# Optimization experiments

Hardware: AMD Instinct MI355X
Metric: run time of the kernel (lower is better)

The kernel has to match this reference:

```python
import jax, jax.numpy as jnp
import numpy as np

N = 50000
L = 3


def gcn_conv(x, W, b, src, dst):
    """PyG-style GCNConv: add self-loops, symmetric deg^-1/2 normalization,
    linear transform, scatter-add aggregation at destination nodes."""
    loops = jnp.arange(N, dtype=src.dtype)
    s = jnp.concatenate([src, loops])  # [E+N]
    d = jnp.concatenate([dst, loops])
    deg = jax.ops.segment_sum(jnp.ones(s.shape[0], x.dtype), d, num_segments=N)
    dinv = jnp.where(deg > 0, jax.lax.rsqrt(deg), jnp.zeros_like(deg))
    norm = dinv[s] * dinv[d]  # [E+N]
    xw = x @ W  # [N, F_out]
    out = jax.ops.segment_sum(xw[s] * norm[:, None], d, num_segments=N)
    return out + b


def setup_inputs() -> dict:
    key = jax.random.key(0)
    ks = jax.random.split(key, 6)
    E = 1600000
    F_in, F_hid, F_out = 256, 128, 64
    x = jax.random.normal(ks[0], (N, F_in), dtype=jnp.float32)
    edges = jax.random.randint(ks[1], (L, 2, E), 0, N, dtype=jnp.int32)
    W1 = jax.random.normal(ks[2], (L, F_in, F_hid), dtype=jnp.float32) * (1.0 / np.sqrt(F_in))
    b1 = jnp.zeros((L, F_hid), dtype=jnp.float32)
    W2 = jax.random.normal(ks[3], (L, F_hid, F_out), dtype=jnp.float32) * (1.0 / np.sqrt(F_hid))
    b2 = jnp.zeros((L, F_out), dtype=jnp.float32)
    return {"x": x, "edges": edges, "W1": W1, "b1": b1, "W2": W2, "b2": b2}


def reference(x, edges, W1, b1, W2, b2):
    # layer 1: sum of L GCNConvs over the L rewired graphs
    h = jnp.zeros((N, W1.shape[2]), dtype=x.dtype)
    for i in range(L):
        h = h + gcn_conv(x, W1[i], b1[i], edges[i, 0], edges[i, 1])
    h = jax.nn.relu(h)
    # layer 2
    out = jnp.zeros((N, W2.shape[2]), dtype=x.dtype)
    for i in range(L):
        out = out + gcn_conv(h, W2[i], b2[i], edges[i, 0], edges[i, 1])
    return out
```

## Files before the change

### kernel.cpp

```cpp
#include <hip/hip_runtime.h>

typedef unsigned int uint;
typedef unsigned short ushort;

#define NN 50000
#define NE 1600000
#define NL 3
#define NB 782
#define CAP 2560
#define CHUNK 8192

typedef float f32x4 __attribute__((ext_vector_type(4)));
typedef __bf16 bf16x4v __attribute__((ext_vector_type(4)));
typedef __bf16 bf16x8v __attribute__((ext_vector_type(8)));

__device__ __forceinline__ ushort f2bf(float f) {
    uint u = __float_as_uint(f);
    u += 0x7fffu + ((u >> 16) & 1u);
    return (ushort)(u >> 16);
}
__device__ __forceinline__ float bf2f(uint lo16) { return __uint_as_float(lo16 << 16); }

__global__ void zero_k(int* __restrict__ p, int n) {
    int i = blockIdx.x * 256 + threadIdx.x;
    if (i < n) p[i] = 0;
}

__global__ void cvt_w(const float* __restrict__ W1, const float* __restrict__ W2,
                      ushort* __restrict__ w1t, ushort* __restrict__ w2t) {
    int idx = blockIdx.x * 256 + threadIdx.x;
    const int n1 = NL * 256 * 128;
    const int n2 = NL * 128 * 64;
    if (idx < n1) {
        int i = idx / (128 * 256);
        int rem = idx % (128 * 256);
        int c = rem / 256, k = rem % 256;
        w1t[idx] = f2bf(W1[i * 256 * 128 + k * 128 + c]);
    } else if (idx < n1 + n2) {
        int j = idx - n1;
        int i = j / (64 * 128);
        int rem = j % (64 * 128);
        int c = rem / 128, k = rem % 128;
        w2t[j] = f2bf(W2[i * 128 * 64 + k * 64 + c]);
    }
}

__global__ __launch_bounds__(256) void bin_edges(const int* __restrict__ edges,
                                                 int* __restrict__ gcur,
                                                 uint* __restrict__ bins) {
    __shared__ uint hist[NB];
    __shared__ uint base[NB];
    const int t = threadIdx.x;
    const int g = blockIdx.y;
    const int e0 = blockIdx.x * CHUNK;
    const int n = min(CHUNK, NE - e0);
    const int* srcp = edges + (size_t)g * 2 * NE;
    const int* dstp = srcp + NE;

    for (int b = t; b < NB; b += 256) hist[b] = 0u;
    __syncthreads();
    for (int k = t; k < n; k += 256) {
        int dst = dstp[e0 + k];
        atomicAdd(&hist[dst >> 6], 1u);
    }
    __syncthreads();
    for (int b = t; b < NB; b += 256) {
        uint cnt = hist[b];
        base[b] = cnt ? (uint)atomicAdd(&gcur[g * NB + b], (int)cnt) : 0u;
        hist[b] = 0u;
    }
    __syncthreads();
    for (int k = t; k < n; k += 256) {
        int dst = dstp[e0 + k];
        int src = srcp[e0 + k];
        int b = dst >> 6;
        uint r = atomicAdd(&hist[b], 1u);
        bins[((size_t)g * NB + b) * CAP + base[b] + r] = ((uint)(dst & 63) << 16) | (uint)src;
    }
}

__global__ __launch_bounds__(256) void csr_bucket(const uint* __restrict__ bins,
                                                  const int* __restrict__ gcur,
                                                  uint* __restrict__ rowse,
                                                  float* __restrict__ dinv,
                                                  ushort* __restrict__ colv16) {
    __shared__ uint h[64];
    __shared__ uint off[64];
    const int t = threadIdx.x;
    const int b = blockIdx.x;
    const int g = blockIdx.y;
    if (t < 64) h[t] = 0u;
    __syncthreads();
    const int n = gcur[g * NB + b];
    const uint* pe = bins + ((size_t)g * NB + b) * CAP;
    for (int k = t; k < n; k += 256) atomicAdd(&h[pe[k] >> 16], 1u);
    __syncthreads();
    if (t < 64) {
        uint cnt = h[t];
        uint x = cnt;
#pragma unroll
        for (int o = 1; o < 64; o <<= 1) {
            uint y = __shfl_up(x, o, 64);
            if (t >= o) x += y;
        }
        uint excl = x - cnt;
        off[t] = excl;
        int v = b * 64 + t;
        if (v < NN) {
            rowse[g * NN + v] = (uint)(b * CAP) + excl | (cnt << 24);
            dinv[g * NN + v] = rsqrtf((float)(cnt + 1));
        }
    }
    __syncthreads();
    if (t < 64) h[t] = off[t];
    __syncthreads();
    ushort* cp = colv16 + (size_t)g * NB * CAP + (size_t)b * CAP;
    for (int k = t; k < n; k += 256) {
        uint e = pe[k];
        uint pos = atomicAdd(&h[e >> 16], 1u);
        cp[pos] = (ushort)(e & 0xffffu);
    }
}

template <int KTOT, int BN, bool QUANT, bool F32A>
__global__ __launch_bounds__(256) void gemm_scaled(const void* __restrict__ Ap,
                                                   const ushort* __restrict__ Bt,
                                                   const float* __restrict__ dinv,
                                                   ushort* __restrict__ OutBf,
                                                   char* __restrict__ OutQ,
                                                   float* __restrict__ OutSc, int M) {
    constexpr int LDT = 72;
    constexpr int NREP = BN / 32;
    __shared__ ushort sA[128 * LDT];
    __shared__ ushort sB[BN * LDT];
    __shared__ float pmax[128][2];
    const int t = threadIdx.x;
    const int lane = t & 63;
    const int wid = t >> 6;
    const int wm = wid >> 1, wn = wid & 1;
    const int by = blockIdx.y;
    const int m0 = blockIdx.x * 128;
    const int sr = t >> 3, sc = t & 7;
    const int lr = lane & 15, lg = lane >> 4;

    f32x4 acc[4][NREP];
#pragma unroll
    for (int m = 0; m < 4; ++m)
#pragma unroll
        for (int n = 0; n < NREP; ++n) acc[m][n] = (f32x4){0.f, 0.f, 0.f, 0.f};

    for (int ks = 0; ks < KTOT / 64; ++ks) {
        __syncthreads();
#pragma unroll
        for (int p = 0; p < 4; ++p) {
            int r = sr + p * 32;
            int grow = m0 + r;
            uint4 val = make_uint4(0u, 0u, 0u, 0u);
            if (grow < M) {
                if constexpr (F32A) {
                    const float* Af = (const float*)Ap;
                    const float4 lo4 =
                        *reinterpret_cast<const float4*>(&Af[(size_t)grow * KTOT + ks * 64 + sc * 8]);
                    const float4 hi4 = *reinterpret_cast<const float4*>(
                        &Af[(size_t)grow * KTOT + ks * 64 + sc * 8 + 4]);
                    val.x = (uint)f2bf(lo4.x) | ((uint)f2bf(lo4.y) << 16);
                    val.y = (uint)f2bf(lo4.z) | ((uint)f2bf(lo4.w) << 16);
                    val.z = (uint)f2bf(hi4.x) | ((uint)f2bf(hi4.y) << 16);
                    val.w = (uint)f2bf(hi4.z) | ((uint)f2bf(hi4.w) << 16);
                } else {
                    const ushort* Ab = (const ushort*)Ap;
                    val = *reinterpret_cast<const uint4*>(&Ab[(size_t)grow * KTOT + ks * 64 + sc * 8]);
                }
            }
            *reinterpret_cast<uint4*>(&sA[r * LDT + sc * 8]) = val;
        }
#pragma unroll
        for (int p = 0; p < BN / 32; ++p) {
            int r = sr + p * 32;
            uint4 val =
                *reinterpret_cast<const uint4*>(&Bt[(size_t)(by * BN + r) * KTOT + ks * 64 + sc * 8]);
            *reinterpret_cast<uint4*>(&sB[r * LDT + sc * 8]) = val;
        }
        __syncthreads();
#pragma unroll
        for (int kk = 0; kk < 2; ++kk) {
            const int kb = kk * 32 + lg * 4;
            bf16x8v af[4], bfr[NREP];
#pragma unroll
            for (int m = 0; m < 4; ++m) {
                const __bf16* p =
                    reinterpret_cast<const __bf16*>(&sA[(wm * 64 + m * 16 + lr) * LDT + kb]);
                bf16x4v lo = *reinterpret_cast<const bf16x4v*>(p);
                bf16x4v hi = *reinterpret_cast<const bf16x4v*>(p + 16);
                af[m] = __builtin_shufflevector(lo, hi, 0, 1, 2, 3, 4, 5, 6, 7);
            }
#pragma unroll
            for (int n = 0; n < NREP; ++n) {
                const __bf16* p =
                    reinterpret_cast<const __bf16*>(&sB[(wn * (BN / 2) + n * 16 + lr) * LDT + kb]);
                bf16x4v lo = *reinterpret_cast<const bf16x4v*>(p);
                bf16x4v hi = *reinterpret_cast<const bf16x4v*>(p + 16);
                bfr[n] = __builtin_shufflevector(lo, hi, 0, 1, 2, 3, 4, 5, 6, 7);
            }
#pragma unroll
            for (int m = 0; m < 4; ++m)
#pragma unroll
                for (int n = 0; n < NREP; ++n)
                    acc[m][n] =
                        __builtin_amdgcn_mfma_f32_16x16x32_bf16(af[m], bfr[n], acc[m][n], 0, 0, 0);
        }
    }
    if constexpr (!QUANT) {
#pragma unroll
        for (int m = 0; m < 4; ++m) {
            int rb = m0 + wm * 64 + m * 16 + lg * 4;
#pragma unroll
            for (int n = 0; n < NREP; ++n) {
                int lcol = wn * (BN / 2) + n * 16 + lr;
#pragma unroll
                for (int r = 0; r < 4; ++r) {
                    int grow = rb + r;
                    if (grow < M) {
                        float v = acc[m][n][r] * dinv[by * NN + grow];
                        OutBf[((size_t)by * M + grow) * BN + lcol] = f2bf(v);
                    }
                }
            }
        }
    } else {
        float pm[4][4];
#pragma unroll
        for (int m = 0; m < 4; ++m)
#pragma unroll
            for (int r = 0; r < 4; ++r) {
                float v = fabsf(acc[m][0][r]);
#pragma unroll
                for (int n = 1; n < NREP; ++n) v = fmaxf(v, fabsf(acc[m][n][r]));
#pragma unroll
                for (int o = 1; o < 16; o <<= 1) v = fmaxf(v, __shfl_xor(v, o, 64));
                pm[m][r] = v;
            }
        if (lr == 0) {
#pragma unroll
            for (int m = 0; m < 4; ++m)
#pragma unroll
                for (int r = 0; r < 4; ++r) pmax[wm * 64 + m * 16 + lg * 4 + r][wn] = pm[m][r];
        }
        __syncthreads();
#pragma unroll
        for (int m = 0; m < 4; ++m) {
#pragma unroll
            for (int r = 0; r < 4; ++r) {
                int brow = wm * 64 + m * 16 + lg * 4 + r;
                int grow = m0 + brow;
                if (grow >= M) continue;
                float mx = fmaxf(pmax[brow][0], pmax[brow][1]);
                float rs = (mx > 0.f) ? 127.f / mx : 0.f;
#pragma unroll
                for (int n = 0; n < NREP; ++n) {
                    int q = (int)rintf(acc[m][n][r] * rs);
                    OutQ[((size_t)by * NN + grow) * BN + wn * (BN / 2) + n * 16 + lr] = (char)q;
                }
                if (wn == 0 && lr == 0)
                    OutSc[by * NN + grow] =
                        (mx > 0.f) ? mx * dinv[by * NN + grow] * (1.f / 127.f) : 0.f;
            }
        }
    }
}

__global__ __launch_bounds__(256) void agg_l1(const ushort* __restrict__ q1,
                                              const float* __restrict__ q1sc,
                                              const ushort* __restrict__ colv16,
                                              const uint* __restrict__ rowse,
                                              const float* __restrict__ b1,
                                              ushort* __restrict__ hout) {
    const int lane = threadIdx.x & 63;
    const int v = blockIdx.x * 4 + (threadIdx.x >> 6);
    float h0 = 0.f, h1 = 0.f;
#pragma unroll
    for (int i = 0; i < NL; ++i) {
        const ushort* tab = q1 + (size_t)i * NN * 64;
        const float* scp = q1sc + i * NN;
        const ushort* cp = colv16 + (size_t)i * NB * CAP;
        uint se = rowse[i * NN + v];
        int e = (int)(se & 0xffffffu);
        int cnt = (int)(se >> 24);
        const int end = e + cnt;
        float dv = rsqrtf((float)(cnt + 1));
        ushort su = tab[(size_t)v * 64 + lane];
        float ssc = scp[v];
        float a0 = ssc * (float)(char)(su & 0xff);
        float a1 = ssc * (float)(char)(su >> 8);
        for (; e + 8 <= end; e += 8) {
            int s0 = cp[e], s1 = cp[e + 1], s2 = cp[e + 2], s3 = cp[e + 3];
            int s4 = cp[e + 4], s5 = cp[e + 5], s6 = cp[e + 6], s7 = cp[e + 7];
            ushort u0 = tab[(size_t)s0 * 64 + lane];
            ushort u1 = tab[(size_t)s1 * 64 + lane];
            ushort u2 = tab[(size_t)s2 * 64 + lane];
            ushort u3 = tab[(size_t)s3 * 64 + lane];
            ushort u4 = tab[(size_t)s4 * 64 + lane];
            ushort u5 = tab[(size_t)s5 * 64 + lane];
            ushort u6 = tab[(size_t)s6 * 64 + lane];
            ushort u7 = tab[(size_t)s7 * 64 + lane];
            float c0 = scp[s0], c1 = scp[s1], c2 = scp[s2], c3 = scp[s3];
            float c4 = scp[s4], c5 = scp[s5], c6 = scp[s6], c7 = scp[s7];
            a0 = fmaf(c0, (float)(char)(u0 & 0xff), a0); a1 = fmaf(c0, (float)(char)(u0 >> 8), a1);
            a0 = fmaf(c1, (float)(char)(u1 & 0xff), a0); a1 = fmaf(c1, (float)(char)(u1 >> 8), a1);
            a0 = fmaf(c2, (float)(char)(u2 & 0xff), a0); a1 = fmaf(c2, (float)(char)(u2 >> 8), a1);
            a0 = fmaf(c3, (float)(char)(u3 & 0xff), a0); a1 = fmaf(c3, (float)(char)(u3 >> 8), a1);
            a0 = fmaf(c4, (float)(char)(u4 & 0xff), a0); a1 = fmaf(c4, (float)(char)(u4 >> 8), a1);
            a0 = fmaf(c5, (float)(char)(u5 & 0xff), a0); a1 = fmaf(c5, (float)(char)(u5 >> 8), a1);
            a0 = fmaf(c6, (float)(char)(u6 & 0xff), a0); a1 = fmaf(c6, (float)(char)(u6 >> 8), a1);
            a0 = fmaf(c7, (float)(char)(u7 & 0xff), a0); a1 = fmaf(c7, (float)(char)(u7 >> 8), a1);
        }
        for (; e < end; ++e) {
            int s = cp[e];
            ushort u = tab[(size_t)s * 64 + lane];
            float c = scp[s];
            a0 = fmaf(c, (float)(char)(u & 0xff), a0);
            a1 = fmaf(c, (float)(char)(u >> 8), a1);
        }
        h0 = fmaf(dv, a0, h0);
        h1 = fmaf(dv, a1, h1);
    }
    int f0 = lane * 2;
    h0 += b1[f0] + b1[128 + f0] + b1[256 + f0];
    h1 += b1[f0 + 1] + b1[128 + f0 + 1] + b1[256 + f0 + 1];
    h0 = fmaxf(h0, 0.f);
    h1 = fmaxf(h1, 0.f);
    uint o = (uint)f2bf(h0) | ((uint)f2bf(h1) << 16);
    reinterpret_cast<uint*>(hout)[(size_t)v * 64 + lane] = o;
}

__global__ __launch_bounds__(256) void agg_l2(const ushort* __restrict__ hw2s,
                                              const ushort* __restrict__ colv16,
                                              const uint* __restrict__ rowse,
                                              const float* __restrict__ b2,
                                              float* __restrict__ out) {
    const int lane = threadIdx.x & 63;
    const int v = blockIdx.x * 4 + (threadIdx.x >> 6);
    float o = 0.f;
#pragma unroll
    for (int i = 0; i < NL; ++i) {
        const ushort* tab = hw2s + (size_t)i * NN * 64;
        const ushort* cp = colv16 + (size_t)i * NB * CAP;
        uint se = rowse[i * NN + v];
        int e = (int)(se & 0xffffffu);
        int cnt = (int)(se >> 24);
        const int end = e + cnt;
        float dv = rsqrtf((float)(cnt + 1));
        float a = bf2f(tab[(size_t)v * 64 + lane]);
        for (; e + 8 <= end; e += 8) {
            int s0 = cp[e], s1 = cp[e + 1], s2 = cp[e + 2], s3 = cp[e + 3];
            int s4 = cp[e + 4], s5 = cp[e + 5], s6 = cp[e + 6], s7 = cp[e + 7];
            float x0 = bf2f(tab[(size_t)s0 * 64 + lane]);
            float x1 = bf2f(tab[(size_t)s1 * 64 + lane]);
            float x2 = bf2f(tab[(size_t)s2 * 64 + lane]);
            float x3 = bf2f(tab[(size_t)s3 * 64 + lane]);
            float x4 = bf2f(tab[(size_t)s4 * 64 + lane]);
            float x5 = bf2f(tab[(size_t)s5 * 64 + lane]);
            float x6 = bf2f(tab[(size_t)s6 * 64 + lane]);
            float x7 = bf2f(tab[(size_t)s7 * 64 + lane]);
            a += ((x0 + x1) + (x2 + x3)) + ((x4 + x5) + (x6 + x7));
        }
        for (; e < end; ++e) a += bf2f(tab[(size_t)cp[e] * 64 + lane]);
        o = fmaf(dv, a, o);
    }
    o += b2[lane] + b2[64 + lane] + b2[128 + lane];
    out[(size_t)v * 64 + lane] = o;
}

extern "C" void kernel_launch(void* const* d_in, const int* in_sizes, int n_in,
                              void* d_out, int out_size, void* d_ws, size_t ws_size,
                              hipStream_t stream) {
    const float* x = (const float*)d_in[0];
    const int* edges = (const int*)d_in[1];
    const float* W1 = (const float*)d_in[2];
    const float* b1 = (const float*)d_in[3];
    const float* W2 = (const float*)d_in[4];
    const float* b2 = (const float*)d_in[5];
    float* out = (float*)d_out;
    char* ws = (char*)d_ws;

    ushort* w1t    = (ushort*)(ws + 0);
    ushort* w2t    = (ushort*)(ws + 196608);
    uint*   rowse  = (uint*)  (ws + 245760);
    float*  q1sc   = (float*) (ws + 845760);
    float*  dinv   = (float*) (ws + 1445760);
    int*    gcur   = (int*)   (ws + 2045760);
    ushort* colv16 = (ushort*)(ws + 2055168);
    uint*   bins   = (uint*)  (ws + 14066688);
    char*   q1     = (char*)  (ws + 38089728);
    ushort* hbf    = (ushort*)(ws + 57289728);
    ushort* hw2s   = (ushort*)(ws + 70089728);

    zero_k<<<dim3((NL * NB + 255) / 256), 256, 0, stream>>>(gcur, NL * NB);
    cvt_w<<<dim3(480), 256, 0, stream>>>(W1, W2, w1t, w2t);

    bin_edges<<<dim3((NE + CHUNK - 1) / CHUNK, NL), 256, 0, stream>>>(edges, gcur, bins);
    csr_bucket<<<dim3(NB, NL), 256, 0, stream>>>(bins, gcur, rowse, dinv, colv16);

    gemm_scaled<256, 128, true, true><<<dim3(391, 3), 256, 0, stream>>>(x, w1t, dinv, nullptr,
                                                                        q1, q1sc, NN);
    agg_l1<<<dim3(NN / 4), 256, 0, stream>>>((const ushort*)q1, q1sc, colv16, rowse, b1, hbf);
    gemm_scaled<128, 64, false, false><<<dim3(391, 3), 256, 0, stream>>>(hbf, w2t, dinv, hw2s,
                                                                         nullptr, nullptr, NN);
    agg_l2<<<dim3(NN / 4), 256, 0, stream>>>(hw2s, colv16, rowse, b2, out);
}
```

Before: 432.0 us.

## Split layer-1 aggregation per graph and feature half with atomic fp32 accumulation

The layer-1 quantized table is stored as separate 64-column halves per graph, and agg_l1 is split into independent blocks per (graph, half, node group). A swizzled block order places blocks that work on the same graph and half close together, so each block's gather footprint is smaller and more likely to stay in cache. Partial results are accumulated into an fp32 buffer with atomicAdd, and the bias plus ReLU are moved into the layer-2 GEMM's A-load path. The cost is an extra zero-fill of a 25.6MB buffer, fp32 atomics, and a larger fp32 read in the second GEMM.

```diff
diff --git a/kernel.cpp b/kernel.cpp
--- a/kernel.cpp
+++ b/kernel.cpp
@@ -9,6 +9,7 @@
 #define NB 782
 #define CAP 2560
 #define CHUNK 8192
+#define NGRP 12500
 
 typedef float f32x4 __attribute__((ext_vector_type(4)));
 typedef __bf16 bf16x4v __attribute__((ext_vector_type(4)));
@@ -27,7 +28,9 @@
 }
 
 __global__ void cvt_w(const float* __restrict__ W1, const float* __restrict__ W2,
-                      ushort* __restrict__ w1t, ushort* __restrict__ w2t) {
+                      const float* __restrict__ b1,
+                      ushort* __restrict__ w1t, ushort* __restrict__ w2t,
+                      float* __restrict__ b1s) {
     int idx = blockIdx.x * 256 + threadIdx.x;
     const int n1 = NL * 256 * 128;
     const int n2 = NL * 128 * 64;
@@ -42,6 +45,9 @@
         int rem = j % (64 * 128);
         int c = rem / 128, k = rem % 128;
         w2t[j] = f2bf(W2[i * 128 * 64 + k * 64 + c]);
+    } else if (idx < n1 + n2 + 128) {
+        int k = idx - n1 - n2;
+        b1s[k] = b1[k] + b1[128 + k] + b1[256 + k];
     }
 }
 
@@ -122,10 +128,11 @@
     }
 }
 
-template <int KTOT, int BN, bool QUANT, bool F32A>
+template <int KTOT, int BN, bool QUANT, bool F32A, bool BRELU>
 __global__ __launch_bounds__(256) void gemm_scaled(const void* __restrict__ Ap,
                                                    const ushort* __restrict__ Bt,
                                                    const float* __restrict__ dinv,
+                                                   const float* __restrict__ b1s,
                                                    ushort* __restrict__ OutBf,
                                                    char* __restrict__ OutQ,
                                                    float* __restrict__ OutSc, int M) {
@@ -159,10 +166,19 @@
             if (grow < M) {
                 if constexpr (F32A) {
                     const float* Af = (const float*)Ap;
-                    const float4 lo4 =
+                    float4 lo4 =
                         *reinterpret_cast<const float4*>(&Af[(size_t)grow * KTOT + ks * 64 + sc * 8]);
-                    const float4 hi4 = *reinterpret_cast<const float4*>(
+                    float4 hi4 = *reinterpret_cast<const float4*>(
                         &Af[(size_t)grow * KTOT + ks * 64 + sc * 8 + 4]);
+                    if constexpr (BRELU) {
+                        const float4 bb0 = *reinterpret_cast<const float4*>(&b1s[ks * 64 + sc * 8]);
+                        const float4 bb1 =
+                            *reinterpret_cast<const float4*>(&b1s[ks * 64 + sc * 8 + 4]);
+                        lo4.x = fmaxf(lo4.x + bb0.x, 0.f); lo4.y = fmaxf(lo4.y + bb0.y, 0.f);
+                        lo4.z = fmaxf(lo4.z + bb0.z, 0.f); lo4.w = fmaxf(lo4.w + bb0.w, 0.f);
+                        hi4.x = fmaxf(hi4.x + bb1.x, 0.f); hi4.y = fmaxf(hi4.y + bb1.y, 0.f);
+                        hi4.z = fmaxf(hi4.z + bb1.z, 0.f); hi4.w = fmaxf(hi4.w + bb1.w, 0.f);
+                    }
                     val.x = (uint)f2bf(lo4.x) | ((uint)f2bf(lo4.y) << 16);
                     val.y = (uint)f2bf(lo4.z) | ((uint)f2bf(lo4.w) << 16);
                     val.z = (uint)f2bf(hi4.x) | ((uint)f2bf(hi4.y) << 16);
@@ -259,7 +275,7 @@
 #pragma unroll
                 for (int n = 0; n < NREP; ++n) {
                     int q = (int)rintf(acc[m][n][r] * rs);
-                    OutQ[((size_t)by * NN + grow) * BN + wn * (BN / 2) + n * 16 + lr] = (char)q;
+                    OutQ[((size_t)(by * 2 + wn) * NN + grow) * 64 + n * 16 + lr] = (char)q;
                 }
                 if (wn == 0 && lr == 0)
                     OutSc[by * NN + grow] =
@@ -269,68 +285,55 @@
     }
 }
 
-__global__ __launch_bounds__(256) void agg_l1(const ushort* __restrict__ q1,
+__global__ __launch_bounds__(256) void agg_l1(const char* __restrict__ q1h,
                                               const float* __restrict__ q1sc,
                                               const ushort* __restrict__ colv16,
                                               const uint* __restrict__ rowse,
-                                              const float* __restrict__ b1,
-                                              ushort* __restrict__ hout) {
+                                              float* __restrict__ h32) {
+    const int b = blockIdx.x;
+    const int unit = (b & 7) * 9375 + (b >> 3);
+    const int combo = unit / NGRP;
+    const int group = unit % NGRP;
+    const int g = combo >> 1;
+    const int hh = combo & 1;
     const int lane = threadIdx.x & 63;
-    const int v = blockIdx.x * 4 + (threadIdx.x >> 6);
-    float h0 = 0.f, h1 = 0.f;
-#pragma unroll
-    for (int i = 0; i < NL; ++i) {
-        const ushort* tab = q1 + (size_t)i * NN * 64;
-        const float* scp = q1sc + i * NN;
-        const ushort* cp = colv16 + (size_t)i * NB * CAP;
-        uint se = rowse[i * NN + v];
-        int e = (int)(se & 0xffffffu);
-        int cnt = (int)(se >> 24);
-        const int end = e + cnt;
-        float dv = rsqrtf((float)(cnt + 1));
-        ushort su = tab[(size_t)v * 64 + lane];
-        float ssc = scp[v];
-        float a0 = ssc * (float)(char)(su & 0xff);
-        float a1 = ssc * (float)(char)(su >> 8);
-        for (; e + 8 <= end; e += 8) {
-            int s0 = cp[e], s1 = cp[e + 1], s2 = cp[e + 2], s3 = cp[e + 3];
-            int s4 = cp[e + 4], s5 = cp[e + 5], s6 = cp[e + 6], s7 = cp[e + 7];
-            ushort u0 = tab[(size_t)s0 * 64 + lane];
-            ushort u1 = tab[(size_t)s1 * 64 + lane];
-            ushort u2 = tab[(size_t)s2 * 64 + lane];
-            ushort u3 = tab[(size_t)s3 * 64 + lane];
-            ushort u4 = tab[(size_t)s4 * 64 + lane];
-            ushort u5 = tab[(size_t)s5 * 64 + lane];
-            ushort u6 = tab[(size_t)s6 * 64 + lane];
-            ushort u7 = tab[(size_t)s7 * 64 + lane];
-            float c0 = scp[s0], c1 = scp[s1], c2 = scp[s2], c3 = scp[s3];
-            float c4 = scp[s4], c5 = scp[s5], c6 = scp[s6], c7 = scp[s7];
-            a0 = fmaf(c0, (float)(char)(u0 & 0xff), a0); a1 = fmaf(c0, (float)(char)(u0 >> 8), a1);
-            a0 = fmaf(c1, (float)(char)(u1 & 0xff), a0); a1 = fmaf(c1, (float)(char)(u1 >> 8), a1);
-            a0 = fmaf(c2, (float)(char)(u2 & 0xff), a0); a1 = fmaf(c2, (float)(char)(u2 >> 8), a1);
-            a0 = fmaf(c3, (float)(char)(u3 & 0xff), a0); a1 = fmaf(c3, (float)(char)(u3 >> 8), a1);
-            a0 = fmaf(c4, (float)(char)(u4 & 0xff), a0); a1 = fmaf(c4, (float)(char)(u4 >> 8), a1);
-            a0 = fmaf(c5, (float)(char)(u5 & 0xff), a0); a1 = fmaf(c5, (float)(char)(u5 >> 8), a1);
-            a0 = fmaf(c6, (float)(char)(u6 & 0xff), a0); a1 = fmaf(c6, (float)(char)(u6 >> 8), a1);
-            a0 = fmaf(c7, (float)(char)(u7 & 0xff), a0); a1 = fmaf(c7, (float)(char)(u7 >> 8), a1);
-        }
-        for (; e < end; ++e) {
-            int s = cp[e];
-            ushort u = tab[(size_t)s * 64 + lane];
-            float c = scp[s];
-            a0 = fmaf(c, (float)(char)(u & 0xff), a0);
-            a1 = fmaf(c, (float)(char)(u >> 8), a1);
-        }
-        h0 = fmaf(dv, a0, h0);
-        h1 = fmaf(dv, a1, h1);
-    }
-    int f0 = lane * 2;
-    h0 += b1[f0] + b1[128 + f0] + b1[256 + f0];
-    h1 += b1[f0 + 1] + b1[128 + f0 + 1] + b1[256 + f0 + 1];
-    h0 = fmaxf(h0, 0.f);
-    h1 = fmaxf(h1, 0.f);
-    uint o = (uint)f2bf(h0) | ((uint)f2bf(h1) << 16);
-    reinterpret_cast<uint*>(hout)[(size_t)v * 64 + lane] = o;
+    const int v = group * 4 + (threadIdx.x >> 6);
+    const char* tab = q1h + (size_t)combo * NN * 64;
+    const float* scp = q1sc + g * NN;
+    const ushort* cp = colv16 + (size_t)g * NB * CAP;
+    uint se = rowse[g * NN + v];
+    int e = (int)(se & 0xffffffu);
+    int cnt = (int)(se >> 24);
+    const int end = e + cnt;
+    float dv = rsqrtf((float)(cnt + 1));
+    float a = scp[v] * (float)tab[(size_t)v * 64 + lane];
+    for (; e + 8 <= end; e += 8) {
+        int s0 = cp[e], s1 = cp[e + 1], s2 = cp[e + 2], s3 = cp[e + 3];
+        int s4 = cp[e + 4], s5 = cp[e + 5], s6 = cp[e + 6], s7 = cp[e + 7];
+        char t0 = tab[(size_t)s0 * 64 + lane];
+        char t1 = tab[(size_t)s1 * 64 + lane];
+        char t2 = tab[(size_t)s2 * 64 + lane];
+        char t3 = tab[(size_t)s3 * 64 + lane];
+        char t4 = tab[(size_t)s4 * 64 + lane];
+        char t5 = tab[(size_t)s5 * 64 + lane];
+        char t6 = tab[(size_t)s6 * 64 + lane];
+        char t7 = tab[(size_t)s7 * 64 + lane];
+        float c0 = scp[s0], c1 = scp[s1], c2 = scp[s2], c3 = scp[s3];
+        float c4 = scp[s4], c5 = scp[s5], c6 = scp[s6], c7 = scp[s7];
+        a = fmaf(c0, (float)t0, a);
+        a = fmaf(c1, (float)t1, a);
+        a = fmaf(c2, (float)t2, a);
+        a = fmaf(c3, (float)t3, a);
+        a = fmaf(c4, (float)t4, a);
+        a = fmaf(c5, (float)t5, a);
+        a = fmaf(c6, (float)t6, a);
+        a = fmaf(c7, (float)t7, a);
+    }
+    for (; e < end; ++e) {
+        int s = cp[e];
+        a = fmaf(scp[s], (float)tab[(size_t)s * 64 + lane], a);
+    }
+    atomicAdd(&h32[(size_t)v * 128 + hh * 64 + lane], dv * a);
 }
 
 __global__ __launch_bounds__(256) void agg_l2(const ushort* __restrict__ hw2s,
@@ -385,26 +388,30 @@
 
     ushort* w1t    = (ushort*)(ws + 0);
     ushort* w2t    = (ushort*)(ws + 196608);
-    uint*   rowse  = (uint*)  (ws + 245760);
-    float*  q1sc   = (float*) (ws + 845760);
-    float*  dinv   = (float*) (ws + 1445760);
-    int*    gcur   = (int*)   (ws + 2045760);
-    ushort* colv16 = (ushort*)(ws + 2055168);
-    uint*   bins   = (uint*)  (ws + 14066688);
-    char*   q1     = (char*)  (ws + 38089728);
-    ushort* hbf    = (ushort*)(ws + 57289728);
-    ushort* hw2s   = (ushort*)(ws + 70089728);
+    float*  b1s    = (float*) (ws + 245760);
+    uint*   rowse  = (uint*)  (ws + 246272);
+    float*  q1sc   = (float*) (ws + 846272);
+    float*  dinv   = (float*) (ws + 1446272);
+    int*    gcur   = (int*)   (ws + 2046272);
+    ushort* colv16 = (ushort*)(ws + 2055680);
+    uint*   bins   = (uint*)  (ws + 14067200);
+    char*   q1h    = (char*)  (ws + 38090240);
+    float*  h32    = (float*) (ws + 57290240);
+    ushort* hw2s   = (ushort*)(ws + 82890240);
 
     zero_k<<<dim3((NL * NB + 255) / 256), 256, 0, stream>>>(gcur, NL * NB);
-    cvt_w<<<dim3(480), 256, 0, stream>>>(W1, W2, w1t, w2t);
+    cvt_w<<<dim3(480), 256, 0, stream>>>(W1, W2, b1, w1t, w2t, b1s);
 
     bin_edges<<<dim3((NE + CHUNK - 1) / CHUNK, NL), 256, 0, stream>>>(edges, gcur, bins);
     csr_bucket<<<dim3(NB, NL), 256, 0, stream>>>(bins, gcur, rowse, dinv, colv16);
 
-    gemm_scaled<256, 128, true, true><<<dim3(391, 3), 256, 0, stream>>>(x, w1t, dinv, nullptr,
-                                                                        q1, q1sc, NN);
-    agg_l1<<<dim3(NN / 4), 256, 0, stream>>>((const ushort*)q1, q1sc, colv16, rowse, b1, hbf);
-    gemm_scaled<128, 64, false, false><<<dim3(391, 3), 256, 0, stream>>>(hbf, w2t, dinv, hw2s,
-                                                                         nullptr, nullptr, NN);
+    gemm_scaled<256, 128, true, true, false><<<dim3(391, 3), 256, 0, stream>>>(
+        x, w1t, dinv, nullptr, nullptr, q1h, q1sc, NN);
+
+    zero_k<<<dim3(NN * 128 / 256), 256, 0, stream>>>((int*)h32, NN * 128);
+    agg_l1<<<dim3(8 * 9375), 256, 0, stream>>>(q1h, q1sc, colv16, rowse, h32);
+
+    gemm_scaled<128, 64, false, true, true><<<dim3(391, 3), 256, 0, stream>>>(
+        h32, w2t, dinv, b1s, hw2s, nullptr, nullptr, NN);
     agg_l2<<<dim3(NN / 4), 256, 0, stream>>>(hw2s, colv16, rowse, b2, out);
 }
```

New measurement: 570.9 us. 32.1% more time.
